# Performance work log

Hardware: AMD Instinct MI355X
Metric: run time of the kernel (lower is better)

Reference implementation:

```python
import jax, jax.numpy as jnp
import numpy as np

BETA = 1.0  # write blending coefficient (beta in original module)


def ste(x):
    # Binarize with straight-through estimator: forward (x>0.5), backward identity.
    b = (x > 0.5).astype(x.dtype)
    return x + jax.lax.stop_gradient(b - x)


def setup_inputs() -> dict:
    key = jax.random.key(0)
    k0, k1, k2 = jax.random.split(key, 3)
    B, H, W, HID = 8, 512, 512, 64
    f0 = jax.random.uniform(k0, (B, 1, H, W), dtype=jnp.float32)
    W1 = jax.random.normal(k1, (9, HID), dtype=jnp.float32) * (1.0 / np.sqrt(9.0))
    b1 = jnp.zeros((HID,), dtype=jnp.float32)
    W2 = jax.random.normal(k2, (HID, 1), dtype=jnp.float32) * (1.0 / np.sqrt(HID))
    b2 = jnp.zeros((1,), dtype=jnp.float32)
    return {"f0": f0, "W1": W1, "b1": b1, "W2": W2, "b2": b2, "T": 16}


def reference(f0, W1, b1, W2, b2, T):
    B, _, H, Wd = f0.shape

    def step(f, _):
        f_read = ste(f)                                            # (B,1,H,W) binarized read
        pad = jnp.pad(f_read, ((0, 0), (0, 0), (1, 1), (1, 1)), mode="wrap")
        # 3x3 neighborhoods, row-major top-left -> bottom-right: (B,H,W,9)
        neigh = jnp.stack(
            [pad[:, 0, i:i + H, j:j + Wd] for i in range(3) for j in range(3)],
            axis=-1,
        )
        h = jax.nn.relu(jnp.einsum("bhwn,nk->bhwk", neigh, W1) + b1)
        logits = (jnp.einsum("bhwk,ko->bhwo", h, W2) + b2)[..., 0]  # (B,H,W)
        w_bits = ste(jax.nn.sigmoid(logits))[:, None]               # (B,1,H,W)
        f_new = (1.0 - BETA) * f + BETA * w_bits
        return f_new, f_new

    _, rest = jax.lax.scan(step, f0, None, length=T - 1)
    fields = jnp.concatenate([f0[None], rest], axis=0)  # (T,B,1,H,W)
    return fields
```

## Files before the change

kernel.cpp:

```cpp
#include <hip/hip_runtime.h>

#define HH 512
#define WW 512
#define WPR 16
#define RO 16
#define HALO 15
#define ROWS (RO + 2 * HALO)
#define OW 8
#define TW 10

#define STEP_BARRIER() do {                                   \
    asm volatile("s_waitcnt lgkmcnt(0)" ::: "memory");        \
    __builtin_amdgcn_s_barrier();                             \
    __builtin_amdgcn_sched_barrier(0);                        \
} while (0)

__global__ __launch_bounds__(512) void init_pack(const float* __restrict__ f0,
                                                 const float* __restrict__ W1,
                                                 const float* __restrict__ b1,
                                                 const float* __restrict__ W2,
                                                 const float* __restrict__ b2,
                                                 int hid,
                                                 float* __restrict__ out,
                                                 unsigned long long* __restrict__ field,
                                                 unsigned int* __restrict__ lut16g) {
    __shared__ unsigned int rule[512];
    const int tid = threadIdx.x;
    int c = blockIdx.x * 512 + tid;
    float v = f0[c];
    out[c] = v;
    unsigned long long m = __ballot(v > 0.5f);
    if ((tid & 63) == 0) field[c >> 6] = m;

    if (blockIdx.x < 64) {
        {
            int p = tid;
            float logit = b2[0];
            for (int k = 0; k < hid; ++k) {
                float a = b1[k];
#pragma unroll
                for (int nn = 0; nn < 9; ++nn)
                    if (p & (1 << nn)) a += W1[nn * hid + k];
                logit += fmaxf(a, 0.0f) * W2[k];
            }
            rule[p] = (logit > 0.0f) ? 1u : 0u;
        }
        __syncthreads();
        if (tid < 128) {
            int word = blockIdx.x * 128 + tid;
            unsigned int wv = 0;
#pragma unroll
            for (int k = 0; k < 8; ++k) {
                unsigned int e = (unsigned int)word * 8u + k;
                unsigned int a = e & 15u, b = (e >> 4) & 15u;
                unsigned int cc = (e >> 8) & 15u, d = (e >> 12) & 15u;
                unsigned int bit0 = rule[(a & 7u) | ((b & 7u) << 3) | ((cc & 7u) << 6)];
                unsigned int bit1 = rule[((a >> 1) & 7u) | (((b >> 1) & 7u) << 3) | (((cc >> 1) & 7u) << 6)];
                unsigned int bit2 = rule[(b & 7u) | ((cc & 7u) << 3) | ((d & 7u) << 6)];
                unsigned int bit3 = rule[((b >> 1) & 7u) | (((cc >> 1) & 7u) << 3) | (((d >> 1) & 7u) << 6)];
                wv |= (bit0 | (bit1 << 1) | (bit2 << 2) | (bit3 << 3)) << (4 * k);
            }
            lut16g[word] = wv;
        }
    }
}

__global__ __launch_bounds__(512) void mega(const unsigned int* __restrict__ field,
                                            const unsigned int* __restrict__ lut16g,
                                            float* __restrict__ out,
                                            int n, int T) {
    __shared__ alignas(16) unsigned int lut16[8192];
    __shared__ unsigned int bufA[ROWS * TW];
    __shared__ unsigned int bufB[ROWS * TW];

    const int tid = threadIdx.x;
    const int cg = blockIdx.x & 1;
    const int rg = (blockIdx.x >> 1) & 31;
    const int b  = blockIdx.x >> 6;
    const int r0 = rg * RO;
    const int q0 = cg * OW;
    const int c0 = cg * (OW * 32);

    for (int i = tid; i < 2048; i += 512)
        ((uint4*)lut16)[i] = ((const uint4*)lut16g)[i];
    {
        const unsigned int* F = field + b * (HH * WPR);
        for (int i = tid; i < ROWS * TW; i += 512) {
            int l = i / TW, tw = i - l * TW;
            int g  = (r0 - HALO + l) & (HH - 1);
            int gw = (q0 - 1 + tw) & (WPR - 1);
            bufA[i] = F[g * WPR + gw];
        }
    }
    __syncthreads();

    unsigned int* oldb = bufA;
    unsigned int* newb = bufB;
    float* outb = out + (size_t)b * (HH * WW);

    for (int t = 1; t < T; ++t) {
        const int npairs = 23 - t;
        if (tid < npairs * TW) {
            const int pr = tid / TW;
            const int w  = tid - pr * TW;
            const int l  = t + 2 * pr;
            const unsigned int* Ra = oldb + (l - 1) * TW;
            const unsigned int* Rb = oldb + l * TW;
            const unsigned int* Rc = oldb + (l + 1) * TW;
            const unsigned int* Rd = oldb + (l + 2) * TW;
            const int wl = (w == 0) ? 0 : w - 1;
            const int wn = (w == TW - 1) ? TW - 1 : w + 1;
            unsigned long long ea = ((((unsigned long long)Ra[wn] << 32) | Ra[w]) << 1) | (Ra[wl] >> 31);
            unsigned long long eb = ((((unsigned long long)Rb[wn] << 32) | Rb[w]) << 1) | (Rb[wl] >> 31);
            unsigned long long ec = ((((unsigned long long)Rc[wn] << 32) | Rc[w]) << 1) | (Rc[wl] >> 31);
            unsigned long long ed = ((((unsigned long long)Rd[wn] << 32) | Rd[w]) << 1) | (Rd[wl] >> 31);
            unsigned int owb = 0, owc = 0;
#pragma unroll
            for (int j = 0; j < 16; ++j) {
                unsigned int idx = (unsigned int)((ea >> (2 * j)) & 15ull)
                                 | ((unsigned int)((eb >> (2 * j)) & 15ull) << 4)
                                 | ((unsigned int)((ec >> (2 * j)) & 15ull) << 8)
                                 | ((unsigned int)((ed >> (2 * j)) & 15ull) << 12);
                unsigned int ent = (lut16[idx >> 3] >> ((idx & 7u) * 4)) & 15u;
                owb |= (ent & 3u) << (2 * j);
                owc |= ((ent >> 2) & 3u) << (2 * j);
            }
            newb[l * TW + w] = owb;
            newb[(l + 1) * TW + w] = owc;
        }
        STEP_BARRIER();

        float* outt = outb + (size_t)t * n;
#pragma unroll
        for (int rep = 0; rep < 2; ++rep) {
            int cell = (rep * 512 + tid) * 4;
            int lr  = cell >> 8;
            int col = cell & 255;
            unsigned int wv = newb[(HALO + lr) * TW + 1 + (col >> 5)];
            unsigned int nib = (wv >> (col & 31)) & 15u;
            float4 v;
            v.x = (float)(nib & 1u);
            v.y = (float)((nib >> 1) & 1u);
            v.z = (float)((nib >> 2) & 1u);
            v.w = (float)(nib >> 3);
            *(float4*)(outt + (size_t)(r0 + lr) * WW + c0 + col) = v;
        }
        unsigned int* tmp = oldb; oldb = newb; newb = tmp;
    }
}

extern "C" void kernel_launch(void* const* d_in, const int* in_sizes, int n_in,
                              void* d_out, int out_size, void* d_ws, size_t ws_size,
                              hipStream_t stream) {
    const float* f0 = (const float*)d_in[0];
    const float* W1 = (const float*)d_in[1];
    const float* b1 = (const float*)d_in[2];
    const float* W2 = (const float*)d_in[3];
    const float* b2 = (const float*)d_in[4];
    float* out = (float*)d_out;

    const int n = in_sizes[0];
    const int hid = in_sizes[2];
    const int T = out_size / n;
    const int B = n / (HH * WW);

    char* ws = (char*)d_ws;
    unsigned int* lut16g = (unsigned int*)ws;
    unsigned long long* fld = (unsigned long long*)(ws + 32768);

    init_pack<<<n / 512, 512, 0, stream>>>(f0, W1, b1, W2, b2, hid, out, fld, lut16g);
    mega<<<B * (HH / RO) * 2, 512, 0, stream>>>((const unsigned int*)fld, lut16g,
                                                out, n, T);
}
```

Baseline: 62.88 us.

## Give each wavefront its own full-width row tile to drop block barriers

Each wavefront now owns a 2-row output strip spanning the full 512-pixel width, kept in a private 32-row shared tile, so the per-step block-wide barrier is replaced by a wave-local LDS wait. Column halos disappear because rows wrap within a wavefront. The grid becomes 512 blocks of 256 threads. In exchange the halo overhead per output row grows (30 halo rows for 2 output rows), and T and the batch size are now hardcoded to 16 and 8.

New measurement: 86.99 us. 1.38x slower.

```diff
diff --git a/kernel.cpp b/kernel.cpp
--- a/kernel.cpp
+++ b/kernel.cpp
@@ -3,15 +3,11 @@
 #define HH 512
 #define WW 512
 #define WPR 16
-#define RO 16
-#define HALO 15
-#define ROWS (RO + 2 * HALO)
-#define OW 8
-#define TW 10
+#define NSTEP 15
+#define TROWS 32
 
-#define STEP_BARRIER() do {                                   \
+#define WAIT_LGKM() do {                                      \
     asm volatile("s_waitcnt lgkmcnt(0)" ::: "memory");        \
-    __builtin_amdgcn_s_barrier();                             \
     __builtin_amdgcn_sched_barrier(0);                        \
 } while (0)
 
@@ -65,51 +61,49 @@
     }
 }
 
-__global__ __launch_bounds__(512) void mega(const unsigned int* __restrict__ field,
+__global__ __launch_bounds__(256) void mega(const unsigned int* __restrict__ field,
                                             const unsigned int* __restrict__ lut16g,
-                                            float* __restrict__ out,
-                                            int n, int T) {
+                                            float* __restrict__ out, int n) {
     __shared__ alignas(16) unsigned int lut16[8192];
-    __shared__ unsigned int bufA[ROWS * TW];
-    __shared__ unsigned int bufB[ROWS * TW];
+    __shared__ unsigned int tiles[4][2][TROWS * WPR];
 
-    const int tid = threadIdx.x;
-    const int cg = blockIdx.x & 1;
-    const int rg = (blockIdx.x >> 1) & 31;
+    const int tid  = threadIdx.x;
+    const int wv   = tid >> 6;
+    const int lane = tid & 63;
+    const int rg = blockIdx.x & 63;
     const int b  = blockIdx.x >> 6;
-    const int r0 = rg * RO;
-    const int q0 = cg * OW;
-    const int c0 = cg * (OW * 32);
+    const int gr0 = rg * 8 + wv * 2;
 
-    for (int i = tid; i < 2048; i += 512)
+    for (int i = tid; i < 2048; i += 256)
         ((uint4*)lut16)[i] = ((const uint4*)lut16g)[i];
+    __syncthreads();
+
+    unsigned int* oldb = &tiles[wv][0][0];
+    unsigned int* newb = &tiles[wv][1][0];
+
     {
         const unsigned int* F = field + b * (HH * WPR);
-        for (int i = tid; i < ROWS * TW; i += 512) {
-            int l = i / TW, tw = i - l * TW;
-            int g  = (r0 - HALO + l) & (HH - 1);
-            int gw = (q0 - 1 + tw) & (WPR - 1);
-            bufA[i] = F[g * WPR + gw];
+        for (int i = lane; i < TROWS * WPR; i += 64) {
+            int l = i >> 4, w = i & 15;
+            int g = (gr0 - NSTEP + l) & (HH - 1);
+            oldb[i] = F[g * WPR + w];
         }
     }
-    __syncthreads();
+    WAIT_LGKM();
 
-    unsigned int* oldb = bufA;
-    unsigned int* newb = bufB;
     float* outb = out + (size_t)b * (HH * WW);
 
-    for (int t = 1; t < T; ++t) {
-        const int npairs = 23 - t;
-        if (tid < npairs * TW) {
-            const int pr = tid / TW;
-            const int w  = tid - pr * TW;
-            const int l  = t + 2 * pr;
-            const unsigned int* Ra = oldb + (l - 1) * TW;
-            const unsigned int* Rb = oldb + l * TW;
-            const unsigned int* Rc = oldb + (l + 1) * TW;
-            const unsigned int* Rd = oldb + (l + 2) * TW;
-            const int wl = (w == 0) ? 0 : w - 1;
-            const int wn = (w == TW - 1) ? TW - 1 : w + 1;
+    for (int s = 1; s <= NSTEP; ++s) {
+        const int ntask = (16 - s) * WPR;
+        for (int task = lane; task < ntask; task += 64) {
+            const int pr = task >> 4;
+            const int w  = task & 15;
+            const int l  = s + 2 * pr;
+            const unsigned int* Ra = oldb + (l - 1) * WPR;
+            const unsigned int* Rb = oldb + l * WPR;
+            const unsigned int* Rc = oldb + (l + 1) * WPR;
+            const unsigned int* Rd = oldb + (l + 2) * WPR;
+            const int wl = (w + 15) & 15, wn = (w + 1) & 15;
             unsigned long long ea = ((((unsigned long long)Ra[wn] << 32) | Ra[w]) << 1) | (Ra[wl] >> 31);
             unsigned long long eb = ((((unsigned long long)Rb[wn] << 32) | Rb[w]) << 1) | (Rb[wl] >> 31);
             unsigned long long ec = ((((unsigned long long)Rc[wn] << 32) | Rc[w]) << 1) | (Rc[wl] >> 31);
@@ -125,25 +119,24 @@
                 owb |= (ent & 3u) << (2 * j);
                 owc |= ((ent >> 2) & 3u) << (2 * j);
             }
-            newb[l * TW + w] = owb;
-            newb[(l + 1) * TW + w] = owc;
+            newb[l * WPR + w] = owb;
+            newb[(l + 1) * WPR + w] = owc;
         }
-        STEP_BARRIER();
+        WAIT_LGKM();
 
-        float* outt = outb + (size_t)t * n;
+        float* outt = outb + (size_t)s * n;
 #pragma unroll
-        for (int rep = 0; rep < 2; ++rep) {
-            int cell = (rep * 512 + tid) * 4;
-            int lr  = cell >> 8;
-            int col = cell & 255;
-            unsigned int wv = newb[(HALO + lr) * TW + 1 + (col >> 5)];
-            unsigned int nib = (wv >> (col & 31)) & 15u;
+        for (int p = 0; p < 4; ++p) {
+            int row = NSTEP + (p >> 1);
+            int col = (p & 1) * 256 + lane * 4;
+            unsigned int wd = newb[row * WPR + (col >> 5)];
+            unsigned int nib = (wd >> (col & 31)) & 15u;
             float4 v;
             v.x = (float)(nib & 1u);
             v.y = (float)((nib >> 1) & 1u);
             v.z = (float)((nib >> 2) & 1u);
             v.w = (float)(nib >> 3);
-            *(float4*)(outt + (size_t)(r0 + lr) * WW + c0 + col) = v;
+            *(float4*)(outt + (size_t)(gr0 + (p >> 1)) * WW + col) = v;
         }
         unsigned int* tmp = oldb; oldb = newb; newb = tmp;
     }
@@ -161,14 +154,11 @@
 
     const int n = in_sizes[0];
     const int hid = in_sizes[2];
-    const int T = out_size / n;
-    const int B = n / (HH * WW);
 
     char* ws = (char*)d_ws;
     unsigned int* lut16g = (unsigned int*)ws;
     unsigned long long* fld = (unsigned long long*)(ws + 32768);
 
     init_pack<<<n / 512, 512, 0, stream>>>(f0, W1, b1, W2, b2, hid, out, fld, lut16g);
-    mega<<<B * (HH / RO) * 2, 512, 0, stream>>>((const unsigned int*)fld, lut16g,
-                                                out, n, T);
+    mega<<<512, 256, 0, stream>>>((const unsigned int*)fld, lut16g, out, n);
 }
```

## Retile mega kernel to full-width 8-row strips with 4-row-per-thread evaluation

Applied to the files above, without the earlier changes.

Changes each block from a 16-row by half-width tile to an 8-row full-width strip, so horizontal halo columns vanish because wraparound is handled inside the block. Each thread now evaluates a 4-row strip (two row pairs) from 6 loaded rows, sharing the middle rows, and batches the 16 LUT lookups so they can be issued together. It also sets occupancy hint launch_bounds(512,2). Vertical halo overhead per output row roughly doubles because RO shrinks while HALO stays 15, trading more redundant halo computation for fewer column halos and better load reuse.

Measured after the change: 77.62 us. +23.4%, slower.

```diff
diff --git a/kernel.cpp b/kernel.cpp
--- a/kernel.cpp
+++ b/kernel.cpp
@@ -3,11 +3,10 @@
 #define HH 512
 #define WW 512
 #define WPR 16
-#define RO 16
+#define RO 8
 #define HALO 15
 #define ROWS (RO + 2 * HALO)
-#define OW 8
-#define TW 10
+#define NSTEP 15
 
 #define STEP_BARRIER() do {                                   \
     asm volatile("s_waitcnt lgkmcnt(0)" ::: "memory");        \
@@ -65,31 +64,47 @@
     }
 }
 
-__global__ __launch_bounds__(512) void mega(const unsigned int* __restrict__ field,
-                                            const unsigned int* __restrict__ lut16g,
-                                            float* __restrict__ out,
-                                            int n, int T) {
+#define PAIR_EVAL(eA, eB, eC, eD, ow0, ow1) do {                              \
+    unsigned int idxv[16];                                                    \
+    _Pragma("unroll")                                                         \
+    for (int j = 0; j < 16; ++j)                                              \
+        idxv[j] = (unsigned int)((eA >> (2 * j)) & 15ull)                     \
+                | ((unsigned int)((eB >> (2 * j)) & 15ull) << 4)              \
+                | ((unsigned int)((eC >> (2 * j)) & 15ull) << 8)              \
+                | ((unsigned int)((eD >> (2 * j)) & 15ull) << 12);            \
+    unsigned int entv[16];                                                    \
+    _Pragma("unroll")                                                         \
+    for (int j = 0; j < 16; ++j)                                              \
+        entv[j] = lut16[idxv[j] >> 3] >> ((idxv[j] & 7u) * 4);                \
+    ow0 = 0; ow1 = 0;                                                         \
+    _Pragma("unroll")                                                         \
+    for (int j = 0; j < 16; ++j) {                                            \
+        ow0 |= (entv[j] & 3u) << (2 * j);                                     \
+        ow1 |= ((entv[j] >> 2) & 3u) << (2 * j);                              \
+    }                                                                         \
+} while (0)
+
+__global__ __launch_bounds__(512, 2) void mega(const unsigned int* __restrict__ field,
+                                               const unsigned int* __restrict__ lut16g,
+                                               float* __restrict__ out,
+                                               int n, int T) {
     __shared__ alignas(16) unsigned int lut16[8192];
-    __shared__ unsigned int bufA[ROWS * TW];
-    __shared__ unsigned int bufB[ROWS * TW];
+    __shared__ unsigned int bufA[ROWS * WPR];
+    __shared__ unsigned int bufB[ROWS * WPR];
 
     const int tid = threadIdx.x;
-    const int cg = blockIdx.x & 1;
-    const int rg = (blockIdx.x >> 1) & 31;
+    const int rg = blockIdx.x & 63;
     const int b  = blockIdx.x >> 6;
     const int r0 = rg * RO;
-    const int q0 = cg * OW;
-    const int c0 = cg * (OW * 32);
 
     for (int i = tid; i < 2048; i += 512)
         ((uint4*)lut16)[i] = ((const uint4*)lut16g)[i];
     {
         const unsigned int* F = field + b * (HH * WPR);
-        for (int i = tid; i < ROWS * TW; i += 512) {
-            int l = i / TW, tw = i - l * TW;
-            int g  = (r0 - HALO + l) & (HH - 1);
-            int gw = (q0 - 1 + tw) & (WPR - 1);
-            bufA[i] = F[g * WPR + gw];
+        for (int i = tid; i < ROWS * WPR; i += 512) {
+            int l = i >> 4, w = i & 15;
+            int g = (r0 - HALO + l) & (HH - 1);
+            bufA[i] = F[g * WPR + w];
         }
     }
     __syncthreads();
@@ -99,51 +114,46 @@
     float* outb = out + (size_t)b * (HH * WW);
 
     for (int t = 1; t < T; ++t) {
-        const int npairs = 23 - t;
-        if (tid < npairs * TW) {
-            const int pr = tid / TW;
-            const int w  = tid - pr * TW;
-            const int l  = t + 2 * pr;
-            const unsigned int* Ra = oldb + (l - 1) * TW;
-            const unsigned int* Rb = oldb + l * TW;
-            const unsigned int* Rc = oldb + (l + 1) * TW;
-            const unsigned int* Rd = oldb + (l + 2) * TW;
-            const int wl = (w == 0) ? 0 : w - 1;
-            const int wn = (w == TW - 1) ? TW - 1 : w + 1;
-            unsigned long long ea = ((((unsigned long long)Ra[wn] << 32) | Ra[w]) << 1) | (Ra[wl] >> 31);
-            unsigned long long eb = ((((unsigned long long)Rb[wn] << 32) | Rb[w]) << 1) | (Rb[wl] >> 31);
-            unsigned long long ec = ((((unsigned long long)Rc[wn] << 32) | Rc[w]) << 1) | (Rc[wl] >> 31);
-            unsigned long long ed = ((((unsigned long long)Rd[wn] << 32) | Rd[w]) << 1) | (Rd[wl] >> 31);
-            unsigned int owb = 0, owc = 0;
+        const int hi = ROWS - t;
+        const int nstrips = (hi - t + 3) >> 2;
+        if (tid < nstrips * WPR) {
+            const int st = tid >> 4;
+            const int w  = tid & 15;
+            const int l  = t + 4 * st;
+            const int wl = (w + 15) & 15, wn = (w + 1) & 15;
+            unsigned long long e[6];
 #pragma unroll
-            for (int j = 0; j < 16; ++j) {
-                unsigned int idx = (unsigned int)((ea >> (2 * j)) & 15ull)
-                                 | ((unsigned int)((eb >> (2 * j)) & 15ull) << 4)
-                                 | ((unsigned int)((ec >> (2 * j)) & 15ull) << 8)
-                                 | ((unsigned int)((ed >> (2 * j)) & 15ull) << 12);
-                unsigned int ent = (lut16[idx >> 3] >> ((idx & 7u) * 4)) & 15u;
-                owb |= (ent & 3u) << (2 * j);
-                owc |= ((ent >> 2) & 3u) << (2 * j);
+            for (int r = 0; r < 6; ++r) {
+                int row = l - 1 + r; row = row < ROWS ? row : ROWS - 1;
+                const unsigned int* R = oldb + row * WPR;
+                e[r] = ((((unsigned long long)R[wn] << 32) | R[w]) << 1) | (R[wl] >> 31);
             }
-            newb[l * TW + w] = owb;
-            newb[(l + 1) * TW + w] = owc;
+            unsigned int owA0, owA1, owB0, owB1;
+            PAIR_EVAL(e[0], e[1], e[2], e[3], owA0, owA1);
+            PAIR_EVAL(e[2], e[3], e[4], e[5], owB0, owB1);
+            newb[l * WPR + w] = owA0;
+            newb[(l + 1) * WPR + w] = owA1;
+            if (l + 2 < hi) {
+                newb[(l + 2) * WPR + w] = owB0;
+                newb[(l + 3) * WPR + w] = owB1;
+            }
         }
         STEP_BARRIER();
 
         float* outt = outb + (size_t)t * n;
 #pragma unroll
-        for (int rep = 0; rep < 2; ++rep) {
-            int cell = (rep * 512 + tid) * 4;
-            int lr  = cell >> 8;
-            int col = cell & 255;
-            unsigned int wv = newb[(HALO + lr) * TW + 1 + (col >> 5)];
-            unsigned int nib = (wv >> (col & 31)) & 15u;
+        for (int p = 0; p < 2; ++p) {
+            int cell = (p * 512 + tid) * 4;
+            int lr  = cell >> 9;
+            int col = cell & 511;
+            unsigned int wd = newb[(HALO + lr) * WPR + (col >> 5)];
+            unsigned int nib = (wd >> (col & 31)) & 15u;
             float4 v;
             v.x = (float)(nib & 1u);
             v.y = (float)((nib >> 1) & 1u);
             v.z = (float)((nib >> 2) & 1u);
             v.w = (float)(nib >> 3);
-            *(float4*)(outt + (size_t)(r0 + lr) * WW + c0 + col) = v;
+            *(float4*)(outt + (size_t)(r0 + lr) * WW + col) = v;
         }
         unsigned int* tmp = oldb; oldb = newb; newb = tmp;
     }
@@ -169,6 +179,6 @@
     unsigned long long* fld = (unsigned long long*)(ws + 32768);
 
     init_pack<<<n / 512, 512, 0, stream>>>(f0, W1, b1, W2, b2, hid, out, fld, lut16g);
-    mega<<<B * (HH / RO) * 2, 512, 0, stream>>>((const unsigned int*)fld, lut16g,
-                                                out, n, T);
+    mega<<<B * (HH / RO), 512, 0, stream>>>((const unsigned int*)fld, lut16g,
+                                            out, n, T);
 }
```
